# Kernel optimization log

Hardware: AMD Instinct MI355X
Metric: run time of the kernel (lower is better)

## Reference

```python
import jax, jax.numpy as jnp
import numpy as np

N_EMBD = 768

def setup_inputs() -> dict:
    key = jax.random.key(0)
    k1, k2, k3, k4 = jax.random.split(key, 4)
    B, T, head_size = 16, 1024, 128
    x = jax.random.normal(k1, (B, T, N_EMBD), dtype=jnp.float32)
    # nn.Linear(in, out, bias=False): weight stored as (out, in); we store transposed (in, out)
    s = 1.0 / np.sqrt(N_EMBD)
    Wk = jax.random.uniform(k2, (N_EMBD, head_size), jnp.float32, -s, s)
    Wq = jax.random.uniform(k3, (N_EMBD, head_size), jnp.float32, -s, s)
    Wv = jax.random.uniform(k4, (N_EMBD, head_size), jnp.float32, -s, s)
    return {"x": x, "Wk": Wk, "Wq": Wq, "Wv": Wv}

def reference(x, Wk, Wq, Wv):
    B, T, C = x.shape  # C == n_embd == 768
    k = jnp.einsum('btc,ch->bth', x, Wk)
    q = jnp.einsum('btc,ch->bth', x, Wq)
    v = jnp.einsum('btc,ch->bth', x, Wv)
    # NOTE: original scales by C**-0.5 with C = n_embd (768), not head_size.
    wei = jnp.einsum('bth,bsh->bts', q, k) * (C ** -0.5)  # (B, T, T)
    causal = jnp.tril(jnp.ones((T, T), dtype=bool))
    wei = jnp.where(causal, wei, -jnp.inf)
    wei = jax.nn.softmax(wei, axis=-1)
    # dropout p=0.0 -> identity
    return jnp.einsum('bts,bsh->bth', wei, v)
```

## Files before the change

### kernel.cpp

```cpp
#include <hip/hip_runtime.h>
#include <hip/hip_bf16.h>
#include <math.h>

#define NTOK   16384
#define NEMBD  768
#define HDIM   128

typedef __attribute__((ext_vector_type(8)))  short short8;
typedef __attribute__((ext_vector_type(16))) float floatx16;

#define MFMA32(a,b,c) __builtin_amdgcn_mfma_f32_32x32x16_bf16(a,b,c,0,0,0)

__device__ __forceinline__ unsigned short f2bf(float f) {
    unsigned u = __float_as_uint(f);
    u += 0x7fff + ((u >> 16) & 1);
    return (unsigned short)(u >> 16);
}
__device__ __forceinline__ unsigned pack2(float a, float b) {
    __hip_bfloat162 h2 = __float22bfloat162_rn(make_float2(a, b));
    union { __hip_bfloat162 h; unsigned u; } c; c.h = h2;
    return c.u;
}
__device__ __forceinline__ unsigned pack2_trunc(float a, float b) {
    return __builtin_amdgcn_perm(__float_as_uint(b), __float_as_uint(a),
                                 0x07060302u);
}
__device__ __forceinline__ void gl_lds16(const void* gptr, void* lptr) {
    __builtin_amdgcn_global_load_lds(
        (const __attribute__((address_space(1))) unsigned int*)gptr,
        (__attribute__((address_space(3))) unsigned int*)lptr, 16, 0, 0);
}

__global__ __launch_bounds__(256) void prep_w(
    const float* __restrict__ Wk, const float* __restrict__ Wq,
    const float* __restrict__ Wv, unsigned short* __restrict__ wt)
{
    __shared__ float T[64 * 65];

    const int tid = threadIdx.x;
    const int bw  = blockIdx.x / 24;
    const int rem = blockIdx.x % 24;
    const int ct  = rem >> 1, dh = rem & 1;
    const int c0  = ct * 64, d0 = dh * 64;
    const float* W = (bw == 0) ? Wk : ((bw == 1) ? Wq : Wv);
    const float scale = (bw == 1)
        ? (0.03608439182435161f * 1.4426950408889634f) : 1.0f;

    #pragma unroll
    for (int pass = 0; pass < 4; ++pass) {
        int idx = pass * 256 + tid;
        int c  = idx >> 4;
        int d4 = idx & 15;
        float4 v = ((const float4*)W)[(size_t)(c0 + c) * 32 + dh * 16 + d4];
        v.x *= scale; v.y *= scale; v.z *= scale; v.w *= scale;
        T[(d4 * 4 + 0) * 65 + c] = v.x;
        T[(d4 * 4 + 1) * 65 + c] = v.y;
        T[(d4 * 4 + 2) * 65 + c] = v.z;
        T[(d4 * 4 + 3) * 65 + c] = v.w;
    }
    __syncthreads();

    #pragma unroll
    for (int pass = 0; pass < 2; ++pass) {
        int idx = pass * 256 + tid;
        int d  = idx >> 3;
        int c8 = idx & 7;
        const float* row = &T[d * 65 + c8 * 8];
        uint4 u = make_uint4(pack2(row[0], row[1]), pack2(row[2], row[3]),
                             pack2(row[4], row[5]), pack2(row[6], row[7]));
        *(uint4*)&wt[(size_t)bw * (HDIM * NEMBD) + (size_t)(d0 + d) * NEMBD
                     + c0 + c8 * 8] = u;
    }
}

__global__ __launch_bounds__(256) void qkv_fused(
    const float* __restrict__ x, const unsigned short* __restrict__ wt,
    unsigned short* __restrict__ kb, unsigned short* __restrict__ qb,
    unsigned short* __restrict__ vT)
{
    __shared__ __align__(16) char As[2][8192];
    __shared__ __align__(16) char Bs[2][16384];

    const int tid = threadIdx.x, w = tid >> 6, lane = tid & 63;
    const int l31 = lane & 31, h = lane >> 5;
    const int r8 = lane >> 3, c8 = lane & 7;
    const int wm = w >> 1, wn = w & 1;
    const int l = blockIdx.x;
    const int low3 = l & 7, rest = l >> 3;
    const int mtile = (rest / 3) * 8 + low3;
    const int nh    = rest % 3;
    const int m0 = mtile * 64;
    const int nbase = nh * 128;
    const int arow = tid >> 2, ac = tid & 3;

    floatx16 acc[2];
    #pragma unroll
    for (int j = 0; j < 2; ++j)
        #pragma unroll
        for (int i = 0; i < 16; ++i) acc[j][i] = 0.f;

    const float* asrc = x + (size_t)(m0 + arow) * NEMBD + ac * 16;

    #pragma unroll
    for (int j = 0; j < 4; ++j) {
        int rowb = w * 32 + j * 8;
        int row  = rowb + r8;
        gl_lds16((const char*)wt + ((size_t)(nbase + row) * NEMBD) * 2
                     + ((c8 ^ (row & 7)) * 16),
                 Bs[0] + rowb * 128);
    }
    float4 a0 = ((const float4*)asrc)[0];
    float4 a1 = ((const float4*)asrc)[1];
    float4 a2 = ((const float4*)asrc)[2];
    float4 a3 = ((const float4*)asrc)[3];
    {
        uint4 u0 = make_uint4(pack2(a0.x, a0.y), pack2(a0.z, a0.w),
                              pack2(a1.x, a1.y), pack2(a1.z, a1.w));
        uint4 u1 = make_uint4(pack2(a2.x, a2.y), pack2(a2.z, a2.w),
                              pack2(a3.x, a3.y), pack2(a3.z, a3.w));
        int cA = 2 * ac, cB = 2 * ac + 1;
        *(uint4*)(As[0] + arow * 128 + ((cA ^ (arow & 7)) * 16)) = u0;
        *(uint4*)(As[0] + arow * 128 + ((cB ^ (arow & 7)) * 16)) = u1;
    }
    {
        const float4* src = (const float4*)(asrc + 64);
        a0 = src[0]; a1 = src[1]; a2 = src[2]; a3 = src[3];
    }
    __syncthreads();

    #pragma unroll
    for (int it = 0; it < 12; ++it) {
        char* Acur = As[it & 1];
        char* Bcur = Bs[it & 1];
        char* Anxt = As[(it & 1) ^ 1];
        char* Bnxt = Bs[(it & 1) ^ 1];

        if (it < 11) {
            const int k0n = (it + 1) * 64;
            #pragma unroll
            for (int j = 0; j < 4; ++j) {
                int rowb = w * 32 + j * 8;
                int row  = rowb + r8;
                gl_lds16((const char*)wt
                             + ((size_t)(nbase + row) * NEMBD + k0n) * 2
                             + ((c8 ^ (row & 7)) * 16),
                         Bnxt + rowb * 128);
            }
        }

        #pragma unroll
        for (int ks = 0; ks < 4; ++ks) {
            int ar = wm * 32 + l31;
            short8 af = *(const short8*)(Acur + ar * 128
                                         + (((2*ks + h) ^ (ar & 7)) * 16));
            #pragma unroll
            for (int j = 0; j < 2; ++j) {
                int br = wn * 64 + j * 32 + l31;
                short8 bf = *(const short8*)(Bcur + br * 128
                                             + (((2*ks + h) ^ (br & 7)) * 16));
                acc[j] = MFMA32(af, bf, acc[j]);
            }
        }

        if (it < 11) {
            uint4 u0 = make_uint4(pack2(a0.x, a0.y), pack2(a0.z, a0.w),
                                  pack2(a1.x, a1.y), pack2(a1.z, a1.w));
            uint4 u1 = make_uint4(pack2(a2.x, a2.y), pack2(a2.z, a2.w),
                                  pack2(a3.x, a3.y), pack2(a3.z, a3.w));
            int cA = 2 * ac, cB = 2 * ac + 1;
            *(uint4*)(Anxt + arow * 128 + ((cA ^ (arow & 7)) * 16)) = u0;
            *(uint4*)(Anxt + arow * 128 + ((cB ^ (arow & 7)) * 16)) = u1;
            if (it < 10) {
                const float4* src = (const float4*)(asrc + (it + 2) * 64);
                a0 = src[0]; a1 = src[1]; a2 = src[2]; a3 = src[3];
            }
        }
        __syncthreads();
    }

    const int tbase = m0 + wm * 32;
    #pragma unroll
    for (int j = 0; j < 2; ++j) {
        int n0loc = wn * 64 + j * 32;
        if (nh < 2) {
            unsigned short* outp = (nh == 0) ? kb : qb;
            int d = n0loc + l31;
            #pragma unroll
            for (int r = 0; r < 16; ++r) {
                int t = tbase + (r & 3) + 8 * (r >> 2) + 4 * h;
                outp[(size_t)t * HDIM + d] = f2bf(acc[j][r]);
            }
        } else {
            int d = n0loc + l31, b = m0 >> 10, tloc = (m0 & 1023) + wm * 32;
            #pragma unroll
            for (int g = 0; g < 4; ++g) {
                int t = tloc + 8 * g + 4 * h;
                uint2 u = make_uint2(pack2(acc[j][4*g+0], acc[j][4*g+1]),
                                     pack2(acc[j][4*g+2], acc[j][4*g+3]));
                *(uint2*)((char*)vT + (((size_t)(b * HDIM + d)) * 1024 + t) * 2) = u;
            }
        }
    }
}

__global__ __launch_bounds__(256) void attn_mfma(
    const unsigned short* __restrict__ qb, const unsigned short* __restrict__ kb,
    const unsigned short* __restrict__ vT, float* __restrict__ out)
{
    __shared__ __align__(16) float Obuf[4 * 32 * 128];
    __shared__ float lred[128];

    const int tid = threadIdx.x, w = tid >> 6, lane = tid & 63;
    const int l31 = lane & 31, h = lane >> 5;
    const int u  = blockIdx.x & 255;
    const int b  = u & 15, p = u >> 4;
    const int qt = (blockIdx.x >> 8) ? (31 - p) : p;

    const char* kb_b = (const char*)kb + (size_t)b * (1024 * 256);
    const char* qb_b = (const char*)qb + (size_t)b * (1024 * 256);
    const char* vT_b = (const char*)vT + (size_t)b * (HDIM * 2048);

    short8 qf[8];
    {
        const char* qrow = qb_b + (size_t)(qt * 32 + l31) * 256 + h * 16;
        #pragma unroll
        for (int ks = 0; ks < 8; ++ks)
            qf[ks] = *(const short8*)(qrow + ks * 32);
    }

    floatx16 o[4];
    #pragma unroll
    for (int nt = 0; nt < 4; ++nt)
        #pragma unroll
        for (int i = 0; i < 16; ++i) o[nt][i] = 0.f;
    float l_r = 0.f;

    short8 kf[8];
    if (w <= qt) {
        const char* krow = kb_b + (size_t)(w * 32 + l31) * 256 + h * 16;
        #pragma unroll
        for (int ks = 0; ks < 8; ++ks)
            kf[ks] = *(const short8*)(krow + ks * 32);
    }

    for (int st = w; st <= qt; st += 4) {
        short8 vf[8];
        {
            const char* vrow0 = vT_b + (size_t)l31 * 2048 + (size_t)st * 64 + h * 16;
            #pragma unroll
            for (int nt = 0; nt < 4; ++nt) {
                const char* vr = vrow0 + (size_t)nt * (32 * 2048);
                vf[nt * 2 + 0] = *(const short8*)(vr + 0);
                vf[nt * 2 + 1] = *(const short8*)(vr + 32);
            }
        }
        floatx16 s;
        #pragma unroll
        for (int i = 0; i < 16; ++i) s[i] = 0.f;
        __builtin_amdgcn_s_setprio(1);
        #pragma unroll
        for (int ks = 0; ks < 8; ++ks) s = MFMA32(kf[ks], qf[ks], s);
        __builtin_amdgcn_s_setprio(0);

        if (st + 4 <= qt) {
            const char* krow = kb_b + (size_t)((st + 4) * 32 + l31) * 256 + h * 16;
            #pragma unroll
            for (int ks = 0; ks < 8; ++ks)
                kf[ks] = *(const short8*)(krow + ks * 32);
        }

        if (st == qt) {
            #pragma unroll
            for (int r = 0; r < 16; ++r) {
                int key = (r & 3) + 8 * (r >> 2) + 4 * h;
                if (key > l31) s[r] = -1e30f;
            }
        }
        float p16[16];
        float ps0 = 0.f, ps1 = 0.f, ps2 = 0.f, ps3 = 0.f;
        #pragma unroll
        for (int r = 0; r < 4; ++r) {
            p16[4*r+0] = __builtin_amdgcn_exp2f(s[4*r+0]);
            p16[4*r+1] = __builtin_amdgcn_exp2f(s[4*r+1]);
            p16[4*r+2] = __builtin_amdgcn_exp2f(s[4*r+2]);
            p16[4*r+3] = __builtin_amdgcn_exp2f(s[4*r+3]);
            ps0 += p16[4*r+0]; ps1 += p16[4*r+1];
            ps2 += p16[4*r+2]; ps3 += p16[4*r+3];
        }
        l_r += (ps0 + ps1) + (ps2 + ps3);

        unsigned own[8];
        #pragma unroll
        for (int i = 0; i < 8; ++i) own[i] = pack2_trunc(p16[2*i], p16[2*i+1]);
        asm("v_permlane32_swap_b32 %0, %1" : "+v"(own[0]), "+v"(own[2]));
        asm("v_permlane32_swap_b32 %0, %1" : "+v"(own[1]), "+v"(own[3]));
        asm("v_permlane32_swap_b32 %0, %1" : "+v"(own[4]), "+v"(own[6]));
        asm("v_permlane32_swap_b32 %0, %1" : "+v"(own[5]), "+v"(own[7]));
        short8 pf[2];
        {
            union { short8 v; unsigned uu[4]; } f0, f1;
            f0.uu[0]=own[0]; f0.uu[1]=own[1]; f0.uu[2]=own[2]; f0.uu[3]=own[3];
            f1.uu[0]=own[4]; f1.uu[1]=own[5]; f1.uu[2]=own[6]; f1.uu[3]=own[7];
            pf[0] = f0.v; pf[1] = f1.v;
        }
        __builtin_amdgcn_s_setprio(1);
        #pragma unroll
        for (int nt = 0; nt < 4; ++nt) {
            o[nt] = MFMA32(vf[nt * 2 + 0], pf[0], o[nt]);
            o[nt] = MFMA32(vf[nt * 2 + 1], pf[1], o[nt]);
        }
        __builtin_amdgcn_s_setprio(0);
    }

    l_r += __shfl_xor(l_r, 32, 64);
    if (lane < 32) lred[w * 32 + l31] = l_r;
    {
        float* mybuf = &Obuf[w * 4096];
        #pragma unroll
        for (int nt = 0; nt < 4; ++nt) {
            #pragma unroll
            for (int g = 0; g < 4; ++g) {
                int chunk = nt * 8 + 2 * g + h;
                int slot  = (chunk & 24) | ((chunk & 7) ^ (l31 & 7));
                *((float4*)&mybuf[l31 * 128] + slot) =
                    make_float4(o[nt][4*g+0], o[nt][4*g+1],
                                o[nt][4*g+2], o[nt][4*g+3]);
            }
        }
    }
    __syncthreads();
    {
        int q  = tid >> 3;
        int cb = (tid & 7) * 4;
        float inv = 1.f / (lred[q] + lred[32 + q] + lred[64 + q] + lred[96 + q]);
        #pragma unroll
        for (int cc = 0; cc < 4; ++cc) {
            int chunk = cb + cc;
            int slot  = (chunk & 24) | ((chunk & 7) ^ (q & 7));
            float4 v0 = *((float4*)&Obuf[0 * 4096 + q * 128] + slot);
            float4 v1 = *((float4*)&Obuf[1 * 4096 + q * 128] + slot);
            float4 v2 = *((float4*)&Obuf[2 * 4096 + q * 128] + slot);
            float4 v3 = *((float4*)&Obuf[3 * 4096 + q * 128] + slot);
            float4 v = make_float4((v0.x + v1.x + v2.x + v3.x) * inv,
                                   (v0.y + v1.y + v2.y + v3.y) * inv,
                                   (v0.z + v1.z + v2.z + v3.z) * inv,
                                   (v0.w + v1.w + v2.w + v3.w) * inv);
            *(float4*)&out[((size_t)(b * 1024 + qt * 32 + q)) * HDIM + chunk * 4] = v;
        }
    }
}

extern "C" void kernel_launch(void* const* d_in, const int* in_sizes, int n_in,
                              void* d_out, int out_size, void* d_ws, size_t ws_size,
                              hipStream_t stream)
{
    const float* x  = (const float*)d_in[0];
    const float* Wk = (const float*)d_in[1];
    const float* Wq = (const float*)d_in[2];
    const float* Wv = (const float*)d_in[3];
    float* outp = (float*)d_out;

    char* ws = (char*)d_ws;
    unsigned short* wt = (unsigned short*)(ws);
    unsigned short* kb = (unsigned short*)(ws + 589824);
    unsigned short* qb = (unsigned short*)(ws + 4784128);
    unsigned short* vT = (unsigned short*)(ws + 8978432);

    prep_w<<<72, 256, 0, stream>>>(Wk, Wq, Wv, wt);
    qkv_fused<<<768, 256, 0, stream>>>(x, wt, kb, qb, vT);
    attn_mfma<<<512, 256, 0, stream>>>(qb, kb, vT, outp);
}
```

Before: 127.1 us.

## Use 512 threads per QKV GEMM block with one 32x32 tile per wave

The QKV projection kernel goes from 4 to 8 waves per block. Each wave now computes a single 32x32 MFMA tile instead of two, and each thread loads half as much A and B data per stage. The A-tile convert-and-store for the next stage is moved ahead of the MFMA loop, so global loads and LDS writes are issued earlier. This is meant to raise latency hiding and memory-level parallelism. In exchange there are more waves per block, more A-fragment reads per MFMA, and higher synchronisation cost per block.

```diff
diff --git a/kernel.cpp b/kernel.cpp
--- a/kernel.cpp
+++ b/kernel.cpp
@@ -73,7 +73,7 @@
     }
 }
 
-__global__ __launch_bounds__(256) void qkv_fused(
+__global__ __launch_bounds__(512) void qkv_fused(
     const float* __restrict__ x, const unsigned short* __restrict__ wt,
     unsigned short* __restrict__ kb, unsigned short* __restrict__ qb,
     unsigned short* __restrict__ vT)
@@ -84,26 +84,24 @@
     const int tid = threadIdx.x, w = tid >> 6, lane = tid & 63;
     const int l31 = lane & 31, h = lane >> 5;
     const int r8 = lane >> 3, c8 = lane & 7;
-    const int wm = w >> 1, wn = w & 1;
+    const int wm = w >> 2, wn = w & 3;
     const int l = blockIdx.x;
     const int low3 = l & 7, rest = l >> 3;
     const int mtile = (rest / 3) * 8 + low3;
     const int nh    = rest % 3;
     const int m0 = mtile * 64;
     const int nbase = nh * 128;
-    const int arow = tid >> 2, ac = tid & 3;
-
-    floatx16 acc[2];
-    #pragma unroll
-    for (int j = 0; j < 2; ++j)
-        #pragma unroll
-        for (int i = 0; i < 16; ++i) acc[j][i] = 0.f;
-
-    const float* asrc = x + (size_t)(m0 + arow) * NEMBD + ac * 16;
-
-    #pragma unroll
-    for (int j = 0; j < 4; ++j) {
-        int rowb = w * 32 + j * 8;
+    const int arow = tid >> 3, ac = tid & 7;
+
+    floatx16 acc;
+    #pragma unroll
+    for (int i = 0; i < 16; ++i) acc[i] = 0.f;
+
+    const float* asrc = x + (size_t)(m0 + arow) * NEMBD + ac * 8;
+
+    #pragma unroll
+    for (int j = 0; j < 2; ++j) {
+        int rowb = w * 16 + j * 8;
         int row  = rowb + r8;
         gl_lds16((const char*)wt + ((size_t)(nbase + row) * NEMBD) * 2
                      + ((c8 ^ (row & 7)) * 16),
@@ -111,20 +109,14 @@
     }
     float4 a0 = ((const float4*)asrc)[0];
     float4 a1 = ((const float4*)asrc)[1];
-    float4 a2 = ((const float4*)asrc)[2];
-    float4 a3 = ((const float4*)asrc)[3];
     {
         uint4 u0 = make_uint4(pack2(a0.x, a0.y), pack2(a0.z, a0.w),
                               pack2(a1.x, a1.y), pack2(a1.z, a1.w));
-        uint4 u1 = make_uint4(pack2(a2.x, a2.y), pack2(a2.z, a2.w),
-                              pack2(a3.x, a3.y), pack2(a3.z, a3.w));
-        int cA = 2 * ac, cB = 2 * ac + 1;
-        *(uint4*)(As[0] + arow * 128 + ((cA ^ (arow & 7)) * 16)) = u0;
-        *(uint4*)(As[0] + arow * 128 + ((cB ^ (arow & 7)) * 16)) = u1;
+        *(uint4*)(As[0] + arow * 128 + ((ac ^ (arow & 7)) * 16)) = u0;
     }
     {
         const float4* src = (const float4*)(asrc + 64);
-        a0 = src[0]; a1 = src[1]; a2 = src[2]; a3 = src[3];
+        a0 = src[0]; a1 = src[1];
     }
     __syncthreads();
 
@@ -138,67 +130,54 @@
         if (it < 11) {
             const int k0n = (it + 1) * 64;
             #pragma unroll
-            for (int j = 0; j < 4; ++j) {
-                int rowb = w * 32 + j * 8;
+            for (int j = 0; j < 2; ++j) {
+                int rowb = w * 16 + j * 8;
                 int row  = rowb + r8;
                 gl_lds16((const char*)wt
                              + ((size_t)(nbase + row) * NEMBD + k0n) * 2
                              + ((c8 ^ (row & 7)) * 16),
                          Bnxt + rowb * 128);
             }
-        }
-
+            uint4 u0 = make_uint4(pack2(a0.x, a0.y), pack2(a0.z, a0.w),
+                                  pack2(a1.x, a1.y), pack2(a1.z, a1.w));
+            *(uint4*)(Anxt + arow * 128 + ((ac ^ (arow & 7)) * 16)) = u0;
+            if (it < 10) {
+                const float4* src = (const float4*)(asrc + (it + 2) * 64);
+                a0 = src[0]; a1 = src[1];
+            }
+        }
+
+        const int ar = wm * 32 + l31;
+        const int br = wn * 32 + l31;
         #pragma unroll
         for (int ks = 0; ks < 4; ++ks) {
-            int ar = wm * 32 + l31;
             short8 af = *(const short8*)(Acur + ar * 128
                                          + (((2*ks + h) ^ (ar & 7)) * 16));
-            #pragma unroll
-            for (int j = 0; j < 2; ++j) {
-                int br = wn * 64 + j * 32 + l31;
-                short8 bf = *(const short8*)(Bcur + br * 128
-                                             + (((2*ks + h) ^ (br & 7)) * 16));
-                acc[j] = MFMA32(af, bf, acc[j]);
-            }
-        }
-
-        if (it < 11) {
-            uint4 u0 = make_uint4(pack2(a0.x, a0.y), pack2(a0.z, a0.w),
-                                  pack2(a1.x, a1.y), pack2(a1.z, a1.w));
-            uint4 u1 = make_uint4(pack2(a2.x, a2.y), pack2(a2.z, a2.w),
-                                  pack2(a3.x, a3.y), pack2(a3.z, a3.w));
-            int cA = 2 * ac, cB = 2 * ac + 1;
-            *(uint4*)(Anxt + arow * 128 + ((cA ^ (arow & 7)) * 16)) = u0;
-            *(uint4*)(Anxt + arow * 128 + ((cB ^ (arow & 7)) * 16)) = u1;
-            if (it < 10) {
-                const float4* src = (const float4*)(asrc + (it + 2) * 64);
-                a0 = src[0]; a1 = src[1]; a2 = src[2]; a3 = src[3];
-            }
+            short8 bf = *(const short8*)(Bcur + br * 128
+                                         + (((2*ks + h) ^ (br & 7)) * 16));
+            acc = MFMA32(af, bf, acc);
         }
         __syncthreads();
     }
 
     const int tbase = m0 + wm * 32;
-    #pragma unroll
-    for (int j = 0; j < 2; ++j) {
-        int n0loc = wn * 64 + j * 32;
-        if (nh < 2) {
-            unsigned short* outp = (nh == 0) ? kb : qb;
-            int d = n0loc + l31;
-            #pragma unroll
-            for (int r = 0; r < 16; ++r) {
-                int t = tbase + (r & 3) + 8 * (r >> 2) + 4 * h;
-                outp[(size_t)t * HDIM + d] = f2bf(acc[j][r]);
-            }
-        } else {
-            int d = n0loc + l31, b = m0 >> 10, tloc = (m0 & 1023) + wm * 32;
-            #pragma unroll
-            for (int g = 0; g < 4; ++g) {
-                int t = tloc + 8 * g + 4 * h;
-                uint2 u = make_uint2(pack2(acc[j][4*g+0], acc[j][4*g+1]),
-                                     pack2(acc[j][4*g+2], acc[j][4*g+3]));
-                *(uint2*)((char*)vT + (((size_t)(b * HDIM + d)) * 1024 + t) * 2) = u;
-            }
+    const int n0loc = wn * 32;
+    if (nh < 2) {
+        unsigned short* outp = (nh == 0) ? kb : qb;
+        int d = n0loc + l31;
+        #pragma unroll
+        for (int r = 0; r < 16; ++r) {
+            int t = tbase + (r & 3) + 8 * (r >> 2) + 4 * h;
+            outp[(size_t)t * HDIM + d] = f2bf(acc[r]);
+        }
+    } else {
+        int d = n0loc + l31, b = m0 >> 10, tloc = (m0 & 1023) + wm * 32;
+        #pragma unroll
+        for (int g = 0; g < 4; ++g) {
+            int t = tloc + 8 * g + 4 * h;
+            uint2 u = make_uint2(pack2(acc[4*g+0], acc[4*g+1]),
+                                 pack2(acc[4*g+2], acc[4*g+3]));
+            *(uint2*)((char*)vT + (((size_t)(b * HDIM + d)) * 1024 + t) * 2) = u;
         }
     }
 }
@@ -367,6 +346,6 @@
     unsigned short* vT = (unsigned short*)(ws + 8978432);
 
     prep_w<<<72, 256, 0, stream>>>(Wk, Wq, Wv, wt);
-    qkv_fused<<<768, 256, 0, stream>>>(x, wt, kb, qb, vT);
+    qkv_fused<<<768, 512, 0, stream>>>(x, wt, kb, qb, vT);
     attn_mfma<<<512, 256, 0, stream>>>(qb, kb, vT, outp);
 }
```

Result: no change. 127.3 us (+0.2%).
